# Kernel optimization log

Hardware: AMD Instinct MI355X
Metric: run time of the kernel (lower is better)

Reference implementation:

```python
import jax, jax.numpy as jnp
import numpy as np

B, NE, E, MULT = 16384, 32, 128, 2
H = MULT * E  # hidden dim per expert


def setup_inputs() -> dict:
    key = jax.random.key(0)
    ks = jax.random.split(key, 6)
    features = jax.random.normal(ks[0], (B, NE, E), dtype=jnp.float32)
    target_features = jax.random.normal(ks[1], (B, NE, E), dtype=jnp.float32)
    # Stacked per-expert params (PyTorch Linear default init scale ~ 1/sqrt(fan_in))
    W1 = jax.random.normal(ks[2], (NE, E, H), dtype=jnp.float32) / np.sqrt(E)
    b1 = jax.random.normal(ks[3], (NE, H), dtype=jnp.float32) * 0.01
    W2 = jax.random.normal(ks[4], (NE, H, E), dtype=jnp.float32) / np.sqrt(H)
    b2 = jax.random.normal(ks[5], (NE, E), dtype=jnp.float32) * 0.01
    return {"features": features, "target_features": target_features,
            "W1": W1, "b1": b1, "W2": W2, "b2": b2}


def reference(features, target_features, W1, b1, W2, b2):
    # Batched grouped MLP over experts: [B, NE, E] x [NE, E, H] -> [B, NE, H]
    h = jnp.einsum('bne,neh->bnh', features, W1) + b1
    h = jax.nn.gelu(h, approximate=False)  # torch nn.GELU default = exact erf
    pred = jnp.einsum('bnh,nhe->bne', h, W2) + b2
    # sum_e mse_loss(pred[:,e], target[:,e]) / NE == mean over all elements
    return jnp.mean((pred - target_features) ** 2)
```

## Files before the change

kernel.cpp:

```cpp
#include <hip/hip_runtime.h>
#include <hip/hip_bf16.h>
#include <math.h>

constexpr int kB  = 16384;
constexpr int kNE = 32;
constexpr int kE  = 128;
constexpr int kH  = 256;

constexpr int MT  = 64;
constexpr int HC  = 64;
constexpr int NCH = kH / HC;

constexpr int SA_S  = kE + 8;
constexpr int SW1_S = kE + 8;
constexpr int SH_S  = HC + 8;
constexpr int SW2_S = HC + 8;

typedef __attribute__((ext_vector_type(8))) short short8;
typedef __attribute__((ext_vector_type(4))) float float4v;

__device__ __forceinline__ unsigned short f2bf(float x) {
  unsigned int u = __float_as_uint(x);
  u += 0x7FFFu + ((u >> 16) & 1u);
  return (unsigned short)(u >> 16);
}

__device__ __forceinline__ float gelu_f(float x) {
  float x2 = x * x;
  float w = x * fmaf(x2, -0.10294428f, -2.30220795f);
  float z = __builtin_amdgcn_exp2f(w);
  return x * __builtin_amdgcn_rcpf(1.0f + z);
}

__global__ __launch_bounds__(256)
void prep_weights(const float* __restrict__ W1, const float* __restrict__ W2,
                  unsigned short* __restrict__ W1T, unsigned short* __restrict__ W2T)
{
  __shared__ unsigned short tile[32][33];
  const int x = threadIdx.x;
  const int y = threadIdx.y;
  int z = blockIdx.z;
  const float* src;
  unsigned short* dst;
  int M, N;
  if (z < kNE) {
    M = kE; N = kH;
    src = W1 + (size_t)z * kE * kH;
    dst = W1T + (size_t)z * kH * kE;
  } else {
    z -= kNE;
    M = kH; N = kE;
    src = W2 + (size_t)z * kH * kE;
    dst = W2T + (size_t)z * kE * kH;
  }
  const int tn = blockIdx.x;
  const int tm = blockIdx.y;
  if (tn * 32 >= N || tm * 32 >= M) return;

#pragma unroll
  for (int r = 0; r < 4; ++r) {
    int row = tm * 32 + y + r * 8;
    int col = tn * 32 + x;
    tile[y + r * 8][x] = f2bf(src[(size_t)row * N + col]);
  }
  __syncthreads();
#pragma unroll
  for (int r = 0; r < 4; ++r) {
    int row = tn * 32 + y + r * 8;
    int col = tm * 32 + x;
    dst[(size_t)row * M + col] = tile[x][y + r * 8];
  }
}

__global__ __launch_bounds__(256)
void distill_moe_mse(const float* __restrict__ features,
                     const float* __restrict__ target,
                     const unsigned short* __restrict__ W1T,
                     const float* __restrict__ b1,
                     const unsigned short* __restrict__ W2T,
                     const float* __restrict__ b2,
                     float* __restrict__ out)
{
  __shared__ __align__(16) unsigned short sA [MT * SA_S];
  __shared__ __align__(16) unsigned short sW1[HC * SW1_S];
  __shared__ __align__(16) unsigned short sH [MT * SH_S];
  __shared__ __align__(16) unsigned short sW2[kE * SW2_S];
  __shared__ float sRed[4];

  const int tid  = threadIdx.x;
  const int lane = tid & 63;
  const int w    = tid >> 6;
  const int q    = lane >> 4;
  const int col  = lane & 15;

  const int n  = blockIdx.y;
  const int b0 = blockIdx.x * MT;

  const int wr = w >> 1;
  const int wc = w & 1;

  const unsigned short* W1n = W1T + (size_t)n * kH * kE;
  const unsigned short* W2n = W2T + (size_t)n * kE * kH;

  float4v accP[2][4];
#pragma unroll
  for (int i = 0; i < 2; ++i)
#pragma unroll
    for (int j = 0; j < 4; ++j)
      accP[i][j] = (float4v){0.f, 0.f, 0.f, 0.f};

  {
    const float* src = features + ((size_t)b0 * kNE + (size_t)n) * kE;
#pragma unroll
    for (int i = 0; i < 4; ++i) {
      int idx = i * 256 + tid;
      int m   = idx >> 4;
      int k   = (idx & 15) << 3;
      const float* p = src + (size_t)m * (kNE * kE) + k;
      float4v f0 = *(const float4v*)(p);
      float4v f1 = *(const float4v*)(p + 4);
      short8 v;
      v[0] = (short)f2bf(f0.x); v[1] = (short)f2bf(f0.y);
      v[2] = (short)f2bf(f0.z); v[3] = (short)f2bf(f0.w);
      v[4] = (short)f2bf(f1.x); v[5] = (short)f2bf(f1.y);
      v[6] = (short)f2bf(f1.z); v[7] = (short)f2bf(f1.w);
      *(short8*)&sA[m * SA_S + k] = v;
    }
  }

  for (int c = 0; c < NCH; ++c) {
    const int hc0 = c * HC;
    __syncthreads();

#pragma unroll
    for (int i = 0; i < 4; ++i) {
      int idx = i * 256 + tid;
      int h   = idx >> 4;
      int kb  = idx & 15;
      short8 v = *(const short8*)(W1n + (size_t)(hc0 + h) * kE + kb * 8);
      *(short8*)&sW1[h * SW1_S + kb * 8] = v;
    }
#pragma unroll
    for (int i = 0; i < 4; ++i) {
      int idx = i * 256 + tid;
      int e   = idx >> 3;
      int hb  = idx & 7;
      short8 v = *(const short8*)(W2n + (size_t)e * kH + hc0 + hb * 8);
      *(short8*)&sW2[e * SW2_S + hb * 8] = v;
    }
    __syncthreads();

    {
      float4v acc[4];
#pragma unroll
      for (int t = 0; t < 4; ++t) acc[t] = (float4v){0.f, 0.f, 0.f, 0.f};
      const int m0 = 16 * w;
#pragma unroll
      for (int kt = 0; kt < 4; ++kt) {
        const int k0 = 32 * kt;
        short8 a = *(const short8*)&sA[(m0 + col) * SA_S + k0 + q * 8];
#pragma unroll
        for (int t = 0; t < 4; ++t) {
          short8 b = *(const short8*)&sW1[(16 * t + col) * SW1_S + k0 + q * 8];
          acc[t] = __builtin_amdgcn_mfma_f32_16x16x32_bf16(a, b, acc[t], 0, 0, 0);
        }
      }
#pragma unroll
      for (int t = 0; t < 4; ++t) {
        float bias = b1[n * kH + hc0 + 16 * t + col];
#pragma unroll
        for (int r = 0; r < 4; ++r) {
          float x = acc[t][r] + bias;
          sH[(m0 + q * 4 + r) * SH_S + 16 * t + col] = f2bf(gelu_f(x));
        }
      }
    }
    __syncthreads();

#pragma unroll
    for (int kt = 0; kt < 2; ++kt) {
      const int k0 = 32 * kt;
      short8 a[2];
#pragma unroll
      for (int i = 0; i < 2; ++i)
        a[i] = *(const short8*)&sH[(32 * wr + 16 * i + col) * SH_S + k0 + q * 8];
#pragma unroll
      for (int j = 0; j < 4; ++j) {
        short8 bf = *(const short8*)&sW2[(64 * wc + 16 * j + col) * SW2_S + k0 + q * 8];
#pragma unroll
        for (int i = 0; i < 2; ++i)
          accP[i][j] = __builtin_amdgcn_mfma_f32_16x16x32_bf16(a[i], bf, accP[i][j], 0, 0, 0);
      }
    }
  }

  {
    float local = 0.f;
#pragma unroll
    for (int j = 0; j < 4; ++j) {
      int e = 64 * wc + 16 * j + col;
      float bias = b2[n * kE + e];
#pragma unroll
      for (int i = 0; i < 2; ++i) {
#pragma unroll
        for (int r = 0; r < 4; ++r) {
          int m = 32 * wr + 16 * i + q * 4 + r;
          float pred = accP[i][j][r] + bias;
          float tgt = target[((size_t)(b0 + m) * kNE + n) * kE + e];
          float d = pred - tgt;
          local += d * d;
        }
      }
    }
#pragma unroll
    for (int off = 32; off > 0; off >>= 1)
      local += __shfl_down(local, off, 64);
    if (lane == 0) sRed[w] = local;
    __syncthreads();
    if (tid == 0) {
      float s = sRed[0] + sRed[1] + sRed[2] + sRed[3];
      atomicAdd(out, s * (1.0f / ((float)kB * (float)kNE * (float)kE)));
    }
  }
}

extern "C" void kernel_launch(void* const* d_in, const int* in_sizes, int n_in,
                              void* d_out, int out_size, void* d_ws, size_t ws_size,
                              hipStream_t stream) {
  const float* features = (const float*)d_in[0];
  const float* target   = (const float*)d_in[1];
  const float* W1       = (const float*)d_in[2];
  const float* b1       = (const float*)d_in[3];
  const float* W2       = (const float*)d_in[4];
  const float* b2       = (const float*)d_in[5];
  float* out = (float*)d_out;

  unsigned short* W1T = (unsigned short*)d_ws;
  unsigned short* W2T = W1T + (size_t)kNE * kH * kE;

  hipMemsetAsync(out, 0, sizeof(float), stream);

  {
    dim3 grid(8, 8, 2 * kNE);
    dim3 block(32, 8);
    prep_weights<<<grid, block, 0, stream>>>(W1, W2, W1T, W2T);
  }
  {
    dim3 grid(kB / MT, kNE);
    dim3 block(256);
    distill_moe_mse<<<grid, block, 0, stream>>>(features, target, W1T, b1, W2T, b2, out);
  }
}
```

Measured before the change: 630.3 us.

## Keep activations in registers, pre-swizzle weights into MFMA fragment layout

After: 574.0 us. -8.9%, faster.

```diff
diff --git a/kernel.cpp b/kernel.cpp
--- a/kernel.cpp
+++ b/kernel.cpp
@@ -1,20 +1,10 @@
 #include <hip/hip_runtime.h>
-#include <hip/hip_bf16.h>
-#include <math.h>
 
 constexpr int kB  = 16384;
 constexpr int kNE = 32;
 constexpr int kE  = 128;
 constexpr int kH  = 256;
-
 constexpr int MT  = 64;
-constexpr int HC  = 64;
-constexpr int NCH = kH / HC;
-
-constexpr int SA_S  = kE + 8;
-constexpr int SW1_S = kE + 8;
-constexpr int SH_S  = HC + 8;
-constexpr int SW2_S = HC + 8;
 
 typedef __attribute__((ext_vector_type(8))) short short8;
 typedef __attribute__((ext_vector_type(4))) float float4v;
@@ -23,6 +13,12 @@
   unsigned int u = __float_as_uint(x);
   u += 0x7FFFu + ((u >> 16) & 1u);
   return (unsigned short)(u >> 16);
+}
+
+__device__ __forceinline__ unsigned int cvt_pk_bf16(float lo, float hi) {
+  unsigned int r;
+  asm("v_cvt_pk_bf16_f32 %0, %1, %2" : "=v"(r) : "v"(lo), "v"(hi));
+  return r;
 }
 
 __device__ __forceinline__ float gelu_f(float x) {
@@ -32,196 +28,172 @@
   return x * __builtin_amdgcn_rcpf(1.0f + z);
 }
 
+__device__ __forceinline__ void load_lds16(const unsigned short* g, unsigned short* l) {
+  __builtin_amdgcn_global_load_lds(
+      (const __attribute__((address_space(1))) unsigned int*)g,
+      (__attribute__((address_space(3))) unsigned int*)l, 16, 0, 0);
+}
+
 __global__ __launch_bounds__(256)
 void prep_weights(const float* __restrict__ W1, const float* __restrict__ W2,
-                  unsigned short* __restrict__ W1T, unsigned short* __restrict__ W2T)
+                  unsigned short* __restrict__ W1F, unsigned short* __restrict__ W2F)
 {
-  __shared__ unsigned short tile[32][33];
-  const int x = threadIdx.x;
-  const int y = threadIdx.y;
-  int z = blockIdx.z;
-  const float* src;
-  unsigned short* dst;
-  int M, N;
-  if (z < kNE) {
-    M = kE; N = kH;
-    src = W1 + (size_t)z * kE * kH;
-    dst = W1T + (size_t)z * kH * kE;
+  const int n    = blockIdx.x;
+  const int lane = threadIdx.x & 63;
+  const int wv   = threadIdx.x >> 6;
+  const int q = lane >> 4, col = lane & 15;
+  const int fb = blockIdx.z * 4 + wv;
+  const int c  = fb >> 4;
+  if (blockIdx.y == 0) {
+    const int kt = (fb >> 2) & 3, t = fb & 3;
+    const float* src = W1 + (size_t)n * kE * kH
+                          + (size_t)(kt * 32 + q * 8) * kH + (c * 64 + t * 16 + col);
+    unsigned short* dst = W1F + (size_t)n * (kH * kE) + ((size_t)fb * 64 + lane) * 8;
+    short8 v;
+#pragma unroll
+    for (int j = 0; j < 8; ++j) v[j] = (short)f2bf(src[(size_t)j * kH]);
+    *(short8*)dst = v;
   } else {
-    z -= kNE;
-    M = kH; N = kE;
-    src = W2 + (size_t)z * kH * kE;
-    dst = W2T + (size_t)z * kE * kH;
-  }
-  const int tn = blockIdx.x;
-  const int tm = blockIdx.y;
-  if (tn * 32 >= N || tm * 32 >= M) return;
-
-#pragma unroll
-  for (int r = 0; r < 4; ++r) {
-    int row = tm * 32 + y + r * 8;
-    int col = tn * 32 + x;
-    tile[y + r * 8][x] = f2bf(src[(size_t)row * N + col]);
-  }
-  __syncthreads();
-#pragma unroll
-  for (int r = 0; r < 4; ++r) {
-    int row = tn * 32 + y + r * 8;
-    int col = tm * 32 + x;
-    dst[(size_t)row * M + col] = tile[x][y + r * 8];
-  }
-}
-
-__global__ __launch_bounds__(256)
+    const int kt = (fb >> 3) & 1, je = fb & 7;
+    const float* src = W2 + (size_t)n * kH * kE
+                          + (size_t)(c * 64 + kt * 32 + q * 8) * kE + (je * 16 + col);
+    unsigned short* dst = W2F + (size_t)n * (kE * kH) + ((size_t)fb * 64 + lane) * 8;
+    short8 v;
+#pragma unroll
+    for (int j = 0; j < 8; ++j) v[j] = (short)f2bf(src[(size_t)j * kE]);
+    *(short8*)dst = v;
+  }
+}
+
+__global__ __launch_bounds__(256, 4)
 void distill_moe_mse(const float* __restrict__ features,
                      const float* __restrict__ target,
-                     const unsigned short* __restrict__ W1T,
+                     const unsigned short* __restrict__ W1F,
                      const float* __restrict__ b1,
-                     const unsigned short* __restrict__ W2T,
+                     const unsigned short* __restrict__ W2F,
                      const float* __restrict__ b2,
                      float* __restrict__ out)
 {
-  __shared__ __align__(16) unsigned short sA [MT * SA_S];
-  __shared__ __align__(16) unsigned short sW1[HC * SW1_S];
-  __shared__ __align__(16) unsigned short sH [MT * SH_S];
-  __shared__ __align__(16) unsigned short sW2[kE * SW2_S];
-  __shared__ float sRed[4];
+  __shared__ __align__(16) unsigned short sW1[8192];
+  __shared__ __align__(16) unsigned short sW2[8192];
 
   const int tid  = threadIdx.x;
   const int lane = tid & 63;
   const int w    = tid >> 6;
   const int q    = lane >> 4;
   const int col  = lane & 15;
-
-  const int n  = blockIdx.y;
-  const int b0 = blockIdx.x * MT;
-
-  const int wr = w >> 1;
-  const int wc = w & 1;
-
-  const unsigned short* W1n = W1T + (size_t)n * kH * kE;
-  const unsigned short* W2n = W2T + (size_t)n * kE * kH;
-
-  float4v accP[2][4];
-#pragma unroll
-  for (int i = 0; i < 2; ++i)
-#pragma unroll
-    for (int j = 0; j < 4; ++j)
-      accP[i][j] = (float4v){0.f, 0.f, 0.f, 0.f};
-
-  {
-    const float* src = features + ((size_t)b0 * kNE + (size_t)n) * kE;
-#pragma unroll
-    for (int i = 0; i < 4; ++i) {
-      int idx = i * 256 + tid;
-      int m   = idx >> 4;
-      int k   = (idx & 15) << 3;
-      const float* p = src + (size_t)m * (kNE * kE) + k;
-      float4v f0 = *(const float4v*)(p);
-      float4v f1 = *(const float4v*)(p + 4);
-      short8 v;
-      v[0] = (short)f2bf(f0.x); v[1] = (short)f2bf(f0.y);
-      v[2] = (short)f2bf(f0.z); v[3] = (short)f2bf(f0.w);
-      v[4] = (short)f2bf(f1.x); v[5] = (short)f2bf(f1.y);
-      v[6] = (short)f2bf(f1.z); v[7] = (short)f2bf(f1.w);
-      *(short8*)&sA[m * SA_S + k] = v;
-    }
-  }
-
-  for (int c = 0; c < NCH; ++c) {
-    const int hc0 = c * HC;
+  const int n    = blockIdx.y;
+  const int m    = blockIdx.x * MT + 16 * w + col;
+
+  const float* arow = features + ((size_t)m * kNE + n) * kE;
+  short8 areg[4];
+#pragma unroll
+  for (int kt = 0; kt < 4; ++kt) {
+    float4v f0 = *(const float4v*)(arow + kt * 32 + q * 8);
+    float4v f1 = *(const float4v*)(arow + kt * 32 + q * 8 + 4);
+    union { unsigned int u[4]; short8 s; } pk;
+    pk.u[0] = cvt_pk_bf16(f0.x, f0.y);
+    pk.u[1] = cvt_pk_bf16(f0.z, f0.w);
+    pk.u[2] = cvt_pk_bf16(f1.x, f1.y);
+    pk.u[3] = cvt_pk_bf16(f1.z, f1.w);
+    areg[kt] = pk.s;
+  }
+
+  float4v acc2[8];
+#pragma unroll
+  for (int je = 0; je < 8; ++je) acc2[je] = (float4v){0.f, 0.f, 0.f, 0.f};
+
+  const unsigned short* W1n = W1F + (size_t)n * (kH * kE);
+  const unsigned short* W2n = W2F + (size_t)n * (kE * kH);
+  const float* b1n = b1 + n * kH;
+
+  for (int c = 0; c < 4; ++c) {
+    if (c) __syncthreads();
+    {
+      const unsigned short* g1 = W1n + c * 8192;
+      const unsigned short* g2 = W2n + c * 8192;
+#pragma unroll
+      for (int i = 0; i < 4; ++i) {
+        int seg = i * 4 + w;
+        load_lds16(g1 + seg * 512 + lane * 8, &sW1[seg * 512]);
+        load_lds16(g2 + seg * 512 + lane * 8, &sW2[seg * 512]);
+      }
+    }
     __syncthreads();
 
-#pragma unroll
-    for (int i = 0; i < 4; ++i) {
-      int idx = i * 256 + tid;
-      int h   = idx >> 4;
-      int kb  = idx & 15;
-      short8 v = *(const short8*)(W1n + (size_t)(hc0 + h) * kE + kb * 8);
-      *(short8*)&sW1[h * SW1_S + kb * 8] = v;
-    }
-#pragma unroll
-    for (int i = 0; i < 4; ++i) {
-      int idx = i * 256 + tid;
-      int e   = idx >> 3;
-      int hb  = idx & 7;
-      short8 v = *(const short8*)(W2n + (size_t)e * kH + hc0 + hb * 8);
-      *(short8*)&sW2[e * SW2_S + hb * 8] = v;
-    }
-    __syncthreads();
-
-    {
-      float4v acc[4];
-#pragma unroll
-      for (int t = 0; t < 4; ++t) acc[t] = (float4v){0.f, 0.f, 0.f, 0.f};
-      const int m0 = 16 * w;
-#pragma unroll
-      for (int kt = 0; kt < 4; ++kt) {
-        const int k0 = 32 * kt;
-        short8 a = *(const short8*)&sA[(m0 + col) * SA_S + k0 + q * 8];
-#pragma unroll
-        for (int t = 0; t < 4; ++t) {
-          short8 b = *(const short8*)&sW1[(16 * t + col) * SW1_S + k0 + q * 8];
-          acc[t] = __builtin_amdgcn_mfma_f32_16x16x32_bf16(a, b, acc[t], 0, 0, 0);
-        }
-      }
+    float4v acc1[4];
+#pragma unroll
+    for (int t = 0; t < 4; ++t) acc1[t] = (float4v){0.f, 0.f, 0.f, 0.f};
+#pragma unroll
+    for (int kt = 0; kt < 4; ++kt) {
 #pragma unroll
       for (int t = 0; t < 4; ++t) {
-        float bias = b1[n * kH + hc0 + 16 * t + col];
-#pragma unroll
-        for (int r = 0; r < 4; ++r) {
-          float x = acc[t][r] + bias;
-          sH[(m0 + q * 4 + r) * SH_S + 16 * t + col] = f2bf(gelu_f(x));
-        }
-      }
-    }
-    __syncthreads();
-
-#pragma unroll
-    for (int kt = 0; kt < 2; ++kt) {
-      const int k0 = 32 * kt;
-      short8 a[2];
-#pragma unroll
-      for (int i = 0; i < 2; ++i)
-        a[i] = *(const short8*)&sH[(32 * wr + 16 * i + col) * SH_S + k0 + q * 8];
-#pragma unroll
-      for (int j = 0; j < 4; ++j) {
-        short8 bf = *(const short8*)&sW2[(64 * wc + 16 * j + col) * SW2_S + k0 + q * 8];
-#pragma unroll
-        for (int i = 0; i < 2; ++i)
-          accP[i][j] = __builtin_amdgcn_mfma_f32_16x16x32_bf16(a[i], bf, accP[i][j], 0, 0, 0);
-      }
-    }
-  }
-
-  {
-    float local = 0.f;
-#pragma unroll
-    for (int j = 0; j < 4; ++j) {
-      int e = 64 * wc + 16 * j + col;
-      float bias = b2[n * kE + e];
-#pragma unroll
-      for (int i = 0; i < 2; ++i) {
-#pragma unroll
-        for (int r = 0; r < 4; ++r) {
-          int m = 32 * wr + 16 * i + q * 4 + r;
-          float pred = accP[i][j][r] + bias;
-          float tgt = target[((size_t)(b0 + m) * kNE + n) * kE + e];
-          float d = pred - tgt;
-          local += d * d;
-        }
-      }
-    }
-#pragma unroll
-    for (int off = 32; off > 0; off >>= 1)
-      local += __shfl_down(local, off, 64);
-    if (lane == 0) sRed[w] = local;
-    __syncthreads();
-    if (tid == 0) {
-      float s = sRed[0] + sRed[1] + sRed[2] + sRed[3];
-      atomicAdd(out, s * (1.0f / ((float)kB * (float)kNE * (float)kE)));
-    }
-  }
+        short8 wf = *(const short8*)&sW1[(kt * 4 + t) * 512 + lane * 8];
+        acc1[t] = __builtin_amdgcn_mfma_f32_16x16x32_bf16(wf, areg[kt], acc1[t], 0, 0, 0);
+      }
+    }
+
+    unsigned int p[4][2];
+    const float* bc = b1n + c * 64;
+#pragma unroll
+    for (int t = 0; t < 4; ++t) {
+      float4v bias = *(const float4v*)(bc + t * 16 + q * 4);
+      float g0 = gelu_f(acc1[t][0] + bias.x);
+      float g1 = gelu_f(acc1[t][1] + bias.y);
+      float g2 = gelu_f(acc1[t][2] + bias.z);
+      float g3 = gelu_f(acc1[t][3] + bias.w);
+      p[t][0] = cvt_pk_bf16(g0, g1);
+      p[t][1] = cvt_pk_bf16(g2, g3);
+    }
+
+    short8 bfrag[2];
+#pragma unroll
+    for (int k2 = 0; k2 < 2; ++k2) {
+      union { unsigned int u[4]; short8 s; } bf;
+#pragma unroll
+      for (int s = 0; s < 2; ++s) {
+        auto uv = __builtin_amdgcn_permlane32_swap(p[2 * k2][s], p[2 * k2 + 1][s], false, false);
+        auto mm = __builtin_amdgcn_permlane16_swap((unsigned int)uv[0], (unsigned int)uv[1], false, false);
+        bf.u[s]     = (unsigned int)mm[0];
+        bf.u[2 + s] = (unsigned int)mm[1];
+      }
+      bfrag[k2] = bf.s;
+    }
+
+#pragma unroll
+    for (int k2 = 0; k2 < 2; ++k2) {
+#pragma unroll
+      for (int je = 0; je < 8; ++je) {
+        short8 wf = *(const short8*)&sW2[(k2 * 8 + je) * 512 + lane * 8];
+        acc2[je] = __builtin_amdgcn_mfma_f32_16x16x32_bf16(wf, bfrag[k2], acc2[je], 0, 0, 0);
+      }
+    }
+  }
+
+  const float* trow = target + ((size_t)m * kNE + n) * kE;
+  const float* b2n  = b2 + n * kE;
+  float local = 0.f;
+#pragma unroll
+  for (int je = 0; je < 8; ++je) {
+    float4v tg = *(const float4v*)(trow + je * 16 + q * 4);
+    float4v bb = *(const float4v*)(b2n + je * 16 + q * 4);
+#pragma unroll
+    for (int r = 0; r < 4; ++r) {
+      float d = acc2[je][r] + bb[r] - tg[r];
+      local += d * d;
+    }
+  }
+#pragma unroll
+  for (int off = 32; off > 0; off >>= 1)
+    local += __shfl_down(local, off, 64);
+
+  __syncthreads();
+  float* sRedF = (float*)sW1;
+  if (lane == 0) sRedF[w] = local;
+  __syncthreads();
+  if (tid == 0)
+    atomicAdd(out, (sRedF[0] + sRedF[1] + sRedF[2] + sRedF[3]) *
+                       (1.0f / ((float)kB * (float)kNE * (float)kE)));
 }
 
 extern "C" void kernel_launch(void* const* d_in, const int* in_sizes, int n_in,
@@ -235,19 +207,17 @@
   const float* b2       = (const float*)d_in[5];
   float* out = (float*)d_out;
 
-  unsigned short* W1T = (unsigned short*)d_ws;
-  unsigned short* W2T = W1T + (size_t)kNE * kH * kE;
+  unsigned short* W1F = (unsigned short*)d_ws;
+  unsigned short* W2F = W1F + (size_t)kNE * kH * kE;
 
   hipMemsetAsync(out, 0, sizeof(float), stream);
 
   {
-    dim3 grid(8, 8, 2 * kNE);
-    dim3 block(32, 8);
-    prep_weights<<<grid, block, 0, stream>>>(W1, W2, W1T, W2T);
+    dim3 grid(kNE, 2, 16);
+    prep_weights<<<grid, dim3(256), 0, stream>>>(W1, W2, W1F, W2F);
   }
   {
     dim3 grid(kB / MT, kNE);
-    dim3 block(256);
-    distill_moe_mse<<<grid, block, 0, stream>>>(features, target, W1T, b1, W2T, b2, out);
-  }
-}
+    distill_moe_mse<<<grid, dim3(256), 0, stream>>>(features, target, W1F, b1, W2F, b2, out);
+  }
+}
```
